# Performance work log

Measured on AMD Instinct MI355X. Metric: run time of the kernel, lower is better.

The kernel has to match this reference:

```python
import jax, jax.numpy as jnp
import numpy as np

EMB = 1024
HEADS = 16
HEAD_DIM = EMB // HEADS
DIM_FF = 4096
EPS = 1e-05


def layer_norm(x, gain, bias):
    # BasicLayerNorm: (x - mean) / (std + eps), std with unbiased=False
    mean = jnp.mean(x, axis=-1, keepdims=True)
    std = jnp.sqrt(jnp.mean((x - mean) ** 2, axis=-1, keepdims=True))
    return gain * ((x - mean) / (std + EPS)) + bias


def setup_inputs() -> dict:
    key = jax.random.key(0)
    ks = jax.random.split(key, 8)
    scale = 1.0 / np.sqrt(EMB)
    x = jax.random.normal(ks[0], (4, 2048, EMB), dtype=jnp.float32)
    Wq = jax.random.normal(ks[1], (EMB, EMB), dtype=jnp.float32) * scale
    Wk = jax.random.normal(ks[2], (EMB, EMB), dtype=jnp.float32) * scale
    Wv = jax.random.normal(ks[3], (EMB, EMB), dtype=jnp.float32) * scale
    Wo = jax.random.normal(ks[4], (EMB, EMB), dtype=jnp.float32) * scale
    W1 = jax.random.normal(ks[5], (EMB, DIM_FF), dtype=jnp.float32) * scale
    b1 = jnp.zeros((DIM_FF,), dtype=jnp.float32)
    W2 = jax.random.normal(ks[6], (DIM_FF, EMB), dtype=jnp.float32) * (1.0 / np.sqrt(DIM_FF))
    b2 = jnp.zeros((EMB,), dtype=jnp.float32)
    gain1 = jnp.ones((EMB,), dtype=jnp.float32)
    bias1 = jnp.zeros((EMB,), dtype=jnp.float32)
    gain2 = jnp.ones((EMB,), dtype=jnp.float32)
    bias2 = jnp.zeros((EMB,), dtype=jnp.float32)
    return dict(x=x, Wq=Wq, Wk=Wk, Wv=Wv, Wo=Wo, W1=W1, b1=b1, W2=W2, b2=b2,
                gain1=gain1, bias1=bias1, gain2=gain2, bias2=bias2)


def reference(x, Wq, Wk, Wv, Wo, W1, b1, W2, b2, gain1, bias1, gain2, bias2):
    b, t, e = x.shape
    h, dk = HEADS, HEAD_DIM
    # QKV projections, split heads -> (b, h, t, dk)
    q = (x @ Wq).reshape(b, t, h, dk).transpose(0, 2, 1, 3)
    k = (x @ Wk).reshape(b, t, h, dk).transpose(0, 2, 1, 3)
    v = (x @ Wv).reshape(b, t, h, dk).transpose(0, 2, 1, 3)
    # scaled dot-product attention
    scores = jnp.einsum('bhqd,bhkd->bhqk', q, k) / jnp.sqrt(jnp.float32(dk))
    attn = jax.nn.softmax(scores, axis=-1)
    ctx = jnp.einsum('bhqk,bhkd->bhqd', attn, v)
    # merge heads and output projection
    merged = ctx.transpose(0, 2, 1, 3).reshape(b, t, e)
    attended = merged @ Wo
    # residual + layer norm 1 (dropout is identity at inference)
    x1 = layer_norm(attended + x, gain1, bias1)
    # feed-forward
    ff = jax.nn.relu(x1 @ W1 + b1) @ W2 + b2
    # residual + layer norm 2
    return layer_norm(ff + x1, gain2, bias2)
```

## Files before the change

### kernel.cpp

```cpp
#include <hip/hip_runtime.h>
#include <hip/hip_bf16.h>
#include <math.h>

#define EMB 1024
#define DIM_FF 4096
#define HEADS 16
#define HD 64
#define TSEQ 2048
#define BATCH 4
#define MROWS (BATCH*TSEQ)
#define LN_EPS 1e-5f

typedef __attribute__((ext_vector_type(8))) short short8;
typedef __attribute__((ext_vector_type(4))) float f32x4;

#define MFMA16(a,b,c) __builtin_amdgcn_mfma_f32_16x16x32_bf16((a),(b),(c),0,0,0)

#define GLOBAL_AS(p) ((const __attribute__((address_space(1))) void*)(p))
#define LDS_AS(p)    ((__attribute__((address_space(3))) void*)(p))

__device__ __forceinline__ unsigned short bf16bits(float f){
    __hip_bfloat16 h = __float2bfloat16(f);
    unsigned short u;
    __builtin_memcpy(&u, &h, 2);
    return u;
}

__global__ __launch_bounds__(256)
void cvt_bf16(const float* __restrict__ in, __hip_bfloat16* __restrict__ out, int n4){
    int i = blockIdx.x*256 + threadIdx.x;
    if (i >= n4) return;
    f32x4 v = reinterpret_cast<const f32x4*>(in)[i];
    union { unsigned short us[4]; uint2 u2; } o;
    #pragma unroll
    for (int j=0;j<4;++j) o.us[j] = bf16bits(v[j]);
    *reinterpret_cast<uint2*>(reinterpret_cast<unsigned short*>(out) + (size_t)i*4) = o.u2;
}

__global__ __launch_bounds__(256)
void transpose_cvt(const float* __restrict__ in, __hip_bfloat16* __restrict__ out, int R, int C){
    __shared__ __hip_bfloat16 tile[32][33];
    int bx = blockIdx.x*32;
    int by = blockIdx.y*32;
    int x = bx + threadIdx.x;
    #pragma unroll
    for (int i = threadIdx.y; i < 32; i += 8){
        tile[i][threadIdx.x] = __float2bfloat16(in[(size_t)(by+i)*C + x]);
    }
    __syncthreads();
    int xo = by + threadIdx.x;
    #pragma unroll
    for (int i = threadIdx.y; i < 32; i += 8){
        out[(size_t)(bx+i)*R + xo] = tile[threadIdx.x][i];
    }
}

template<int EPI>
__global__ __launch_bounds__(256, 2)
void gemm_bt(const __hip_bfloat16* __restrict__ A,
             const __hip_bfloat16* __restrict__ Bt,
             int M, int N, int K,
             float* __restrict__ Cf,
             __hip_bfloat16* __restrict__ Cb,
             const float* __restrict__ bias,
             __hip_bfloat16* __restrict__ qo,
             __hip_bfloat16* __restrict__ ko,
             __hip_bfloat16* __restrict__ vto)
{
    __shared__ __align__(16) __hip_bfloat16 As[128*32];
    __shared__ __align__(16) __hip_bfloat16 Bs[128*32];
    const int tid = threadIdx.x;
    const int lane = tid & 63;
    const int wid = tid >> 6;
    const int wm = wid >> 1, wn = wid & 1;
    const int row0 = blockIdx.x * 128;
    const int col0 = blockIdx.y * 128;
    const int rA = lane & 15, kg = lane >> 4;

    const int lrow = lane >> 2;
    const int lcol = (lane & 3) << 3;

    f32x4 acc[4][4] = {};

    for (int kt = 0; kt < K; kt += 32) {
        __syncthreads();
        #pragma unroll
        for (int half = 0; half < 2; ++half) {
            const int rbase = (wid << 5) + (half << 4);
            const int r = rbase + lrow;
            __builtin_amdgcn_global_load_lds(
                GLOBAL_AS(A + (size_t)(row0 + r)*K + kt + lcol),
                LDS_AS(&As[rbase*32]), 16, 0, 0);
            __builtin_amdgcn_global_load_lds(
                GLOBAL_AS(Bt + (size_t)(col0 + r)*K + kt + lcol),
                LDS_AS(&Bs[rbase*32]), 16, 0, 0);
        }
        __syncthreads();
        short8 af[4], bfr[4];
        #pragma unroll
        for (int mi = 0; mi < 4; ++mi)
            af[mi] = *reinterpret_cast<const short8*>(&As[(wm*64 + mi*16 + rA)*32 + (kg<<3)]);
        #pragma unroll
        for (int ni = 0; ni < 4; ++ni)
            bfr[ni] = *reinterpret_cast<const short8*>(&Bs[(wn*64 + ni*16 + rA)*32 + (kg<<3)]);
        #pragma unroll
        for (int mi = 0; mi < 4; ++mi)
            #pragma unroll
            for (int ni = 0; ni < 4; ++ni)
                acc[mi][ni] = MFMA16(af[mi], bfr[ni], acc[mi][ni]);
    }

    #pragma unroll
    for (int mi=0; mi<4; ++mi) {
        #pragma unroll
        for (int ni=0; ni<4; ++ni) {
            #pragma unroll
            for (int j=0;j<4;++j){
                float v = acc[mi][ni][j];
                int grow = row0 + wm*64 + mi*16 + (kg<<2) + j;
                int gcol = col0 + wn*64 + ni*16 + rA;
                if constexpr (EPI==0) {
                    int b = grow >> 11, t = grow & 2047;
                    int which = gcol >> 10, hdx = gcol & 1023;
                    int h = hdx >> 6, d = hdx & 63;
                    int bh = b*HEADS + h;
                    __hip_bfloat16 bv = __float2bfloat16(v);
                    if (which==0)      qo[((size_t)bh*TSEQ + t)*HD + d] = bv;
                    else if (which==1) ko[((size_t)bh*TSEQ + t)*HD + d] = bv;
                    else               vto[((size_t)bh*HD + d)*TSEQ + t] = bv;
                } else if constexpr (EPI==1) {
                    Cf[(size_t)grow*N + gcol] = v;
                } else if constexpr (EPI==2) {
                    v += bias[gcol]; v = v > 0.0f ? v : 0.0f;
                    Cb[(size_t)grow*N + gcol] = __float2bfloat16(v);
                } else {
                    Cf[(size_t)grow*N + gcol] = v + bias[gcol];
                }
            }
        }
    }
}

__global__ __launch_bounds__(256, 4)
void attn_fwd(const __hip_bfloat16* __restrict__ q,
              const __hip_bfloat16* __restrict__ k,
              const __hip_bfloat16* __restrict__ vt,
              __hip_bfloat16* __restrict__ merged)
{
    const int wg = (blockIdx.x & 7) * 256 + (blockIdx.x >> 3);
    const int bh = wg >> 5;
    const int qt = wg & 31;
    const int wid = threadIdx.x >> 6, lane = threadIdx.x & 63;
    const int rA = lane & 15, kg = lane >> 4;
    const int qrow0 = qt*64 + wid*16;
    const __hip_bfloat16* Qh = q  + (size_t)bh*TSEQ*HD;
    const __hip_bfloat16* Kh = k  + (size_t)bh*TSEQ*HD;
    const __hip_bfloat16* Vh = vt + (size_t)bh*HD*TSEQ;

    __shared__ __align__(16) __hip_bfloat16 Kl[2][64*64];
    __shared__ __align__(16) __hip_bfloat16 Vl[2][64*64];
    __shared__ __align__(16) __hip_bfloat16 plds[4][8][16][8];

    short8 aQ0 = *reinterpret_cast<const short8*>(Qh + (size_t)(qrow0+rA)*HD + (kg<<3));
    short8 aQ1 = *reinterpret_cast<const short8*>(Qh + (size_t)(qrow0+rA)*HD + 32 + (kg<<3));

    const int lrow = lane >> 3;
    const int lslot = ((lane & 7) ^ lrow) << 3;
    const __hip_bfloat16* sK0 = Kh + (size_t)(wid*16 + lrow)*HD + lslot;
    const __hip_bfloat16* sV0 = Vh + (size_t)(wid*16 + lrow)*TSEQ + lslot;
    const int dOff = wid*16*64;

    f32x4 O[4] = {};
    float m = -1e30f, l = 0.f;
    const int swz = rA & 7;

    {
        __builtin_amdgcn_global_load_lds(GLOBAL_AS(sK0),          LDS_AS(&Kl[0][dOff]),        16, 0, 0);
        __builtin_amdgcn_global_load_lds(GLOBAL_AS(sK0 + 8*HD),   LDS_AS(&Kl[0][dOff + 8*64]), 16, 0, 0);
        __builtin_amdgcn_global_load_lds(GLOBAL_AS(sV0),          LDS_AS(&Vl[0][dOff]),        16, 0, 0);
        __builtin_amdgcn_global_load_lds(GLOBAL_AS(sV0 + 8*TSEQ), LDS_AS(&Vl[0][dOff + 8*64]), 16, 0, 0);
    }
    __syncthreads();

    for (int t = 0; t < TSEQ/64; ++t) {
        const int b = t & 1;
        if (t < TSEQ/64 - 1) {
            const int kt = (t+1)*64;
            __builtin_amdgcn_global_load_lds(GLOBAL_AS(sK0 + (size_t)kt*HD),          LDS_AS(&Kl[b^1][dOff]),        16, 0, 0);
            __builtin_amdgcn_global_load_lds(GLOBAL_AS(sK0 + (size_t)(kt+8)*HD),      LDS_AS(&Kl[b^1][dOff + 8*64]), 16, 0, 0);
            __builtin_amdgcn_global_load_lds(GLOBAL_AS(sV0 + kt),                     LDS_AS(&Vl[b^1][dOff]),        16, 0, 0);
            __builtin_amdgcn_global_load_lds(GLOBAL_AS(sV0 + 8*TSEQ + kt),            LDS_AS(&Vl[b^1][dOff + 8*64]), 16, 0, 0);
        }
        const char* Kb = (const char*)&Kl[b][0];
        const char* Vb = (const char*)&Vl[b][0];

        f32x4 st[4];
        #pragma unroll
        for (int kb = 0; kb < 4; ++kb) {
            const int ro = (kb*16 + rA) * 128;
            short8 aK0 = *reinterpret_cast<const short8*>(Kb + ro + ((kg ^ swz) << 4));
            short8 aK1 = *reinterpret_cast<const short8*>(Kb + ro + (((4+kg) ^ swz) << 4));
            f32x4 z = {};
            z = MFMA16(aK0, aQ0, z);
            st[kb] = MFMA16(aK1, aQ1, z);
        }
        f32x4 sm01, sm;
        #pragma unroll
        for (int j=0;j<4;++j) sm01[j] = fmaxf(st[0][j], st[1][j]);
        #pragma unroll
        for (int j=0;j<4;++j) sm[j] = fmaxf(sm01[j], fmaxf(st[2][j], st[3][j]));
        float mx = fmaxf(fmaxf(sm[0], sm[1]), fmaxf(sm[2], sm[3]));
        mx = fmaxf(mx, __shfl_xor(mx, 16));
        mx = fmaxf(mx, __shfl_xor(mx, 32));
        float mn = fmaxf(m, mx*0.125f);
        float al = __expf(m - mn);
        f32x4 ps[4];
        #pragma unroll
        for (int kb=0; kb<4; ++kb)
            #pragma unroll
            for (int j=0;j<4;++j)
                ps[kb][j] = __expf(fmaf(st[kb][j], 0.125f, -mn));
        f32x4 ssv = (ps[0]+ps[1]) + (ps[2]+ps[3]);
        float rs = (ssv[0]+ssv[1]) + (ssv[2]+ssv[3]);
        rs += __shfl_xor(rs, 16);
        rs += __shfl_xor(rs, 32);
        l = l*al + rs; m = mn;
        float alq[4];
        #pragma unroll
        for (int j=0;j<4;++j) alq[j] = __shfl(al, (kg<<2)+j);
        #pragma unroll
        for (int dt=0; dt<4; ++dt)
            #pragma unroll
            for (int j=0;j<4;++j) O[dt][j] *= alq[j];
        #pragma unroll
        for (int kb=0; kb<4; ++kb) {
            uint2 w;
            w.x = (unsigned)bf16bits(ps[kb][0]) | ((unsigned)bf16bits(ps[kb][1]) << 16);
            w.y = (unsigned)bf16bits(ps[kb][2]) | ((unsigned)bf16bits(ps[kb][3]) << 16);
            *reinterpret_cast<uint2*>(&plds[wid][2*kb + (kg>>1)][rA][(kg&1)<<2]) = w;
        }
        short8 aP0 = *reinterpret_cast<const short8*>(&plds[wid][kg][rA][0]);
        short8 aP1 = *reinterpret_cast<const short8*>(&plds[wid][4+kg][rA][0]);
        #pragma unroll
        for (int dt=0; dt<4; ++dt) {
            const int vo = (dt*16 + rA) * 128;
            short8 bV0 = *reinterpret_cast<const short8*>(Vb + vo + ((kg ^ swz) << 4));
            short8 bV1 = *reinterpret_cast<const short8*>(Vb + vo + (((4+kg) ^ swz) << 4));
            O[dt] = MFMA16(aP0, bV0, O[dt]);
            O[dt] = MFMA16(aP1, bV1, O[dt]);
        }
        __syncthreads();
    }

    float lq[4];
    #pragma unroll
    for (int j=0;j<4;++j) lq[j] = 1.0f / __shfl(l, (kg<<2)+j);
    const int b = bh >> 4, h = bh & 15;
    #pragma unroll
    for (int dt=0; dt<4; ++dt){
        #pragma unroll
        for (int j=0;j<4;++j){
            int t = qrow0 + (kg<<2) + j;
            int col = h*HD + dt*16 + rA;
            merged[((size_t)(b*TSEQ + t))*EMB + col] = __float2bfloat16(O[dt][j]*lq[j]);
        }
    }
}

__global__ __launch_bounds__(256)
void ln_res(const float* __restrict__ a, const float* __restrict__ res,
            const float* __restrict__ gain, const float* __restrict__ bias,
            float* __restrict__ outf, __hip_bfloat16* __restrict__ outb)
{
    const int row = blockIdx.x;
    const int tid = threadIdx.x;
    const int lane = tid & 63, wid = tid >> 6;
    const size_t base = (size_t)row * EMB;
    f32x4 va = *reinterpret_cast<const f32x4*>(a + base + tid*4);
    f32x4 vr = *reinterpret_cast<const f32x4*>(res + base + tid*4);
    f32x4 v = va + vr;
    float s = v[0]+v[1]+v[2]+v[3];
    #pragma unroll
    for (int off=1; off<64; off<<=1) s += __shfl_xor(s, off);
    __shared__ float red1[4], red2[4];
    if (lane==0) red1[wid] = s;
    __syncthreads();
    float mean = (red1[0]+red1[1]+red1[2]+red1[3]) * (1.0f/EMB);
    f32x4 d;
    #pragma unroll
    for (int j=0;j<4;++j) d[j] = v[j] - mean;
    float qs = d[0]*d[0]+d[1]*d[1]+d[2]*d[2]+d[3]*d[3];
    #pragma unroll
    for (int off=1; off<64; off<<=1) qs += __shfl_xor(qs, off);
    if (lane==0) red2[wid] = qs;
    __syncthreads();
    float var = (red2[0]+red2[1]+red2[2]+red2[3]) * (1.0f/EMB);
    float r = 1.0f/(sqrtf(var)+LN_EPS);
    f32x4 g = *reinterpret_cast<const f32x4*>(gain + tid*4);
    f32x4 bb = *reinterpret_cast<const f32x4*>(bias + tid*4);
    f32x4 o;
    #pragma unroll
    for (int j=0;j<4;++j) o[j] = g[j]*(d[j]*r) + bb[j];
    *reinterpret_cast<f32x4*>(outf + base + tid*4) = o;
    if (outb) {
        union { unsigned short us[4]; uint2 u2; } ob;
        #pragma unroll
        for (int j=0;j<4;++j) ob.us[j] = bf16bits(o[j]);
        *reinterpret_cast<uint2*>(reinterpret_cast<unsigned short*>(outb) + base + tid*4) = ob.u2;
    }
}

extern "C" void kernel_launch(void* const* d_in, const int* in_sizes, int n_in,
                              void* d_out, int out_size, void* d_ws, size_t ws_size,
                              hipStream_t stream) {
    const float* x   = (const float*)d_in[0];
    const float* Wq  = (const float*)d_in[1];
    const float* Wk  = (const float*)d_in[2];
    const float* Wv  = (const float*)d_in[3];
    const float* Wo  = (const float*)d_in[4];
    const float* W1  = (const float*)d_in[5];
    const float* b1  = (const float*)d_in[6];
    const float* W2  = (const float*)d_in[7];
    const float* b2  = (const float*)d_in[8];
    const float* gain1 = (const float*)d_in[9];
    const float* bias1 = (const float*)d_in[10];
    const float* gain2 = (const float*)d_in[11];
    const float* bias2 = (const float*)d_in[12];

    char* ws = (char*)d_ws;
    __hip_bfloat16* Wqkv_t = (__hip_bfloat16*)(ws + 0);
    __hip_bfloat16* Wo_t   = (__hip_bfloat16*)(ws + 6291456);
    __hip_bfloat16* W1_t   = (__hip_bfloat16*)(ws + 8388608);
    __hip_bfloat16* W2_t   = (__hip_bfloat16*)(ws + 16777216);
    __hip_bfloat16* xb     = (__hip_bfloat16*)(ws + 25165824);
    __hip_bfloat16* qb     = (__hip_bfloat16*)(ws + 41943040);
    __hip_bfloat16* kb     = (__hip_bfloat16*)(ws + 58720256);
    __hip_bfloat16* vtb    = (__hip_bfloat16*)(ws + 75497472);
    __hip_bfloat16* h1     = (__hip_bfloat16*)(ws + 25165824);
    __hip_bfloat16* mergedb= (__hip_bfloat16*)(ws + 92274688);
    float*          attended=(float*)(ws + 109051904);
    float*          ff     = (float*)(ws + 92274688);
    float*          x1f    = (float*)(ws + 142606336);
    __hip_bfloat16* x1b    = (__hip_bfloat16*)(ws + 176160768);
    float*          outf   = (float*)d_out;

    dim3 tb(32,8);
    transpose_cvt<<<dim3(32,32),  tb, 0, stream>>>(Wq, Wqkv_t,                 1024, 1024);
    transpose_cvt<<<dim3(32,32),  tb, 0, stream>>>(Wk, Wqkv_t + 1024*1024,     1024, 1024);
    transpose_cvt<<<dim3(32,32),  tb, 0, stream>>>(Wv, Wqkv_t + 2*1024*1024,   1024, 1024);
    transpose_cvt<<<dim3(32,32),  tb, 0, stream>>>(Wo, Wo_t,                   1024, 1024);
    transpose_cvt<<<dim3(128,32), tb, 0, stream>>>(W1, W1_t,                   1024, 4096);
    transpose_cvt<<<dim3(32,128), tb, 0, stream>>>(W2, W2_t,                   4096, 1024);
    cvt_bf16<<<(MROWS*EMB/4 + 255)/256, 256, 0, stream>>>(x, xb, MROWS*EMB/4);

    gemm_bt<0><<<dim3(MROWS/128, 3072/128), 256, 0, stream>>>(
        xb, Wqkv_t, MROWS, 3072, EMB, nullptr, nullptr, nullptr, qb, kb, vtb);
    attn_fwd<<<dim3(2048), 256, 0, stream>>>(qb, kb, vtb, mergedb);
    gemm_bt<1><<<dim3(MROWS/128, EMB/128), 256, 0, stream>>>(
        mergedb, Wo_t, MROWS, EMB, EMB, attended, nullptr, nullptr, nullptr, nullptr, nullptr);
    ln_res<<<MROWS, 256, 0, stream>>>(attended, x, gain1, bias1, x1f, x1b);
    gemm_bt<2><<<dim3(MROWS/128, DIM_FF/128), 256, 0, stream>>>(
        x1b, W1_t, MROWS, DIM_FF, EMB, nullptr, h1, b1, nullptr, nullptr, nullptr);
    gemm_bt<3><<<dim3(MROWS/128, EMB/128), 256, 0, stream>>>(
        h1, W2_t, MROWS, EMB, DIM_FF, ff, nullptr, b2, nullptr, nullptr, nullptr);
    ln_res<<<MROWS, 256, 0, stream>>>(ff, x1f, gain2, bias2, outf, nullptr);
}
```

Before: 486.9 us.

## Add 256x256 double-buffered GEMM with direct global-to-LDS loads for QKV and FFN1

Result: no change. 487.7 us (+0.2%).

```diff
diff --git a/kernel.cpp b/kernel.cpp
--- a/kernel.cpp
+++ b/kernel.cpp
@@ -61,11 +61,7 @@
              const __hip_bfloat16* __restrict__ Bt,
              int M, int N, int K,
              float* __restrict__ Cf,
-             __hip_bfloat16* __restrict__ Cb,
-             const float* __restrict__ bias,
-             __hip_bfloat16* __restrict__ qo,
-             __hip_bfloat16* __restrict__ ko,
-             __hip_bfloat16* __restrict__ vto)
+             const float* __restrict__ bias)
 {
     __shared__ __align__(16) __hip_bfloat16 As[128*32];
     __shared__ __align__(16) __hip_bfloat16 Bs[128*32];
@@ -119,6 +115,117 @@
                 float v = acc[mi][ni][j];
                 int grow = row0 + wm*64 + mi*16 + (kg<<2) + j;
                 int gcol = col0 + wn*64 + ni*16 + rA;
+                if constexpr (EPI==1) {
+                    Cf[(size_t)grow*N + gcol] = v;
+                } else {
+                    Cf[(size_t)grow*N + gcol] = v + bias[gcol];
+                }
+            }
+        }
+    }
+}
+
+#define GPHASE(P, STAGE_EXPR, WAIT_EXPR) do { \
+    short8 af[2][2]; \
+    _Pragma("unroll") \
+    for (int i_=0;i_<2;++i_){ \
+      _Pragma("unroll") \
+      for (int kk_=0;kk_<2;++kk_) \
+        af[i_][kk_] = *reinterpret_cast<const short8*>(pA + ((2*(P)+i_)*16+rA)*128 + (((kk_<<2)+kg)^swz)*16); \
+    } \
+    STAGE_EXPR; WAIT_EXPR; \
+    __builtin_amdgcn_s_barrier(); \
+    __builtin_amdgcn_s_setprio(1); \
+    _Pragma("unroll") \
+    for (int i_=0;i_<2;++i_){ \
+      _Pragma("unroll") \
+      for (int ni_=0;ni_<4;++ni_){ \
+        acc[2*(P)+i_][ni_] = MFMA16(af[i_][0], bfr[ni_][0], acc[2*(P)+i_][ni_]); \
+        acc[2*(P)+i_][ni_] = MFMA16(af[i_][1], bfr[ni_][1], acc[2*(P)+i_][ni_]); \
+      } \
+    } \
+    __builtin_amdgcn_s_setprio(0); \
+    __builtin_amdgcn_s_barrier(); \
+} while(0)
+
+template<int EPI>
+__global__ __launch_bounds__(512, 2)
+void gemm256(const __hip_bfloat16* __restrict__ A,
+             const __hip_bfloat16* __restrict__ Bt,
+             int M, int N, int K,
+             __hip_bfloat16* __restrict__ Cb,
+             const float* __restrict__ bias,
+             __hip_bfloat16* __restrict__ qo,
+             __hip_bfloat16* __restrict__ ko,
+             __hip_bfloat16* __restrict__ vto)
+{
+    __shared__ __align__(16) __hip_bfloat16 Al[2][16384];
+    __shared__ __align__(16) __hip_bfloat16 Bl[2][16384];
+    const int tid = threadIdx.x;
+    const int lane = tid & 63;
+    const int wid = tid >> 6;
+    const int wm = wid >> 2, wn = wid & 3;
+    const int row0 = blockIdx.x * 256;
+    const int col0 = blockIdx.y * 256;
+    const int rA = lane & 15, kg = lane >> 4, swz = rA & 7;
+    const int NT = K >> 6;
+
+    const int lr = lane >> 3;
+    const int lg = (lane & 7) ^ lr;
+    const __hip_bfloat16* sA = A  + (size_t)(row0 + wid*8 + lr)*K + lg*8;
+    const __hip_bfloat16* sB = Bt + (size_t)(col0 + wid*8 + lr)*K + lg*8;
+    char* dA = (char*)&Al[0][0] + wid*8*128;
+    char* dB = (char*)&Bl[0][0] + wid*8*128;
+
+    auto stage = [&](const __hip_bfloat16* s, char* d, int buf, int half, int kt){
+        #pragma unroll
+        for (int rr = 0; rr < 2; ++rr)
+            __builtin_amdgcn_global_load_lds(
+                GLOBAL_AS(s + (size_t)(half*128 + rr*64)*K + kt),
+                LDS_AS(d + buf*32768 + (half*128 + rr*64)*128), 16, 0, 0);
+    };
+
+    f32x4 acc[8][4] = {};
+
+    stage(sA, dA, 0, 0, 0); stage(sA, dA, 0, 1, 0);
+    stage(sB, dB, 0, 0, 0); stage(sB, dB, 0, 1, 0);
+    stage(sB, dB, 1, 0, 64); stage(sB, dB, 1, 1, 64);
+    asm volatile("s_waitcnt vmcnt(4)" ::: "memory");
+    __builtin_amdgcn_sched_barrier(0);
+    __builtin_amdgcn_s_barrier();
+
+    const char* cA = (const char*)&Al[0][0] + wm*128*128;
+    const char* cB = (const char*)&Bl[0][0] + wn*64*128;
+
+    for (int t = 0; t < NT; ++t) {
+        const int buf = t & 1;
+        const char* pA = cA + buf*32768;
+        const char* pB = cB + buf*32768;
+        short8 bfr[4][2];
+        #pragma unroll
+        for (int ni = 0; ni < 4; ++ni)
+            #pragma unroll
+            for (int kk = 0; kk < 2; ++kk)
+                bfr[ni][kk] = *reinterpret_cast<const short8*>(pB + (ni*16+rA)*128 + (((kk<<2)+kg)^swz)*16);
+
+        GPHASE(0, if (t+1 < NT) stage(sA, dA, buf^1, 0, (t+1)*64), );
+        GPHASE(1, if (t+1 < NT) stage(sA, dA, buf^1, 1, (t+1)*64), );
+        GPHASE(2, if (t+2 < NT) stage(sB, dB, buf,   0, (t+2)*64), );
+        GPHASE(3, if (t+2 < NT) stage(sB, dB, buf,   1, (t+2)*64),
+            if (t+2 < NT) { asm volatile("s_waitcnt vmcnt(4)" ::: "memory"); }
+            else          { asm volatile("s_waitcnt vmcnt(0)" ::: "memory"); }
+            __builtin_amdgcn_sched_barrier(0) );
+    }
+
+    #pragma unroll
+    for (int mi=0; mi<8; ++mi) {
+        #pragma unroll
+        for (int ni=0; ni<4; ++ni) {
+            #pragma unroll
+            for (int j=0;j<4;++j){
+                float v = acc[mi][ni][j];
+                int grow = row0 + wm*128 + mi*16 + (kg<<2) + j;
+                int gcol = col0 + wn*64 + ni*16 + rA;
                 if constexpr (EPI==0) {
                     int b = grow >> 11, t = grow & 2047;
                     int which = gcol >> 10, hdx = gcol & 1023;
@@ -128,13 +235,9 @@
                     if (which==0)      qo[((size_t)bh*TSEQ + t)*HD + d] = bv;
                     else if (which==1) ko[((size_t)bh*TSEQ + t)*HD + d] = bv;
                     else               vto[((size_t)bh*HD + d)*TSEQ + t] = bv;
-                } else if constexpr (EPI==1) {
-                    Cf[(size_t)grow*N + gcol] = v;
-                } else if constexpr (EPI==2) {
+                } else {
                     v += bias[gcol]; v = v > 0.0f ? v : 0.0f;
                     Cb[(size_t)grow*N + gcol] = __float2bfloat16(v);
-                } else {
-                    Cf[(size_t)grow*N + gcol] = v + bias[gcol];
                 }
             }
         }
@@ -353,15 +456,15 @@
     transpose_cvt<<<dim3(32,128), tb, 0, stream>>>(W2, W2_t,                   4096, 1024);
     cvt_bf16<<<(MROWS*EMB/4 + 255)/256, 256, 0, stream>>>(x, xb, MROWS*EMB/4);
 
-    gemm_bt<0><<<dim3(MROWS/128, 3072/128), 256, 0, stream>>>(
-        xb, Wqkv_t, MROWS, 3072, EMB, nullptr, nullptr, nullptr, qb, kb, vtb);
+    gemm256<0><<<dim3(MROWS/256, 3072/256), 512, 0, stream>>>(
+        xb, Wqkv_t, MROWS, 3072, EMB, nullptr, nullptr, qb, kb, vtb);
     attn_fwd<<<dim3(2048), 256, 0, stream>>>(qb, kb, vtb, mergedb);
     gemm_bt<1><<<dim3(MROWS/128, EMB/128), 256, 0, stream>>>(
-        mergedb, Wo_t, MROWS, EMB, EMB, attended, nullptr, nullptr, nullptr, nullptr, nullptr);
+        mergedb, Wo_t, MROWS, EMB, EMB, attended, nullptr);
     ln_res<<<MROWS, 256, 0, stream>>>(attended, x, gain1, bias1, x1f, x1b);
-    gemm_bt<2><<<dim3(MROWS/128, DIM_FF/128), 256, 0, stream>>>(
-        x1b, W1_t, MROWS, DIM_FF, EMB, nullptr, h1, b1, nullptr, nullptr, nullptr);
+    gemm256<2><<<dim3(MROWS/256, DIM_FF/256), 512, 0, stream>>>(
+        x1b, W1_t, MROWS, DIM_FF, EMB, h1, b1, nullptr, nullptr, nullptr);
     gemm_bt<3><<<dim3(MROWS/128, EMB/128), 256, 0, stream>>>(
-        h1, W2_t, MROWS, EMB, DIM_FF, ff, nullptr, b2, nullptr, nullptr, nullptr);
+        h1, W2_t, MROWS, EMB, DIM_FF, ff, b2);
     ln_res<<<MROWS, 256, 0, stream>>>(ff, x1f, gain2, bias2, outf, nullptr);
 }
```
